# Kernel optimization log

Measured on AMD Instinct MI355X. Metric: run time of the kernel, lower is better.

Reference implementation:

```python
import jax, jax.numpy as jnp
import numpy as np

B, D = 128, 512
ORDER, DEPTH = 1, 2


def setup_inputs() -> dict:
    key = jax.random.key(0)
    kx, kw = jax.random.split(key)
    x = jax.random.normal(kx, (B, D), dtype=jnp.float32)
    # scale the cubic meta-weight so repeated contractions stay O(1)
    W = jax.random.normal(kw, (D, D, D), dtype=jnp.float32) * (1.0 / np.sqrt(D))
    bias = jnp.zeros((D,), dtype=jnp.float32)
    return {"x": x, "W": W, "bias": bias}


def reference(x, W, bias):
    # Meta-linear: per-sample effective weight obtained by contracting the
    # trailing `ORDER` modes of W (out, in, in, ...) with x, rescaled by
    # 1/sqrt(d) per contraction, then applied as a linear layer; repeat DEPTH times.
    sqrt_d = np.sqrt(x.shape[-1]).astype(np.float32)
    for _ in range(DEPTH):
        # first contraction introduces the batch dim: (out, in, k) x (b, k) -> (b, out, in)
        w = jnp.einsum('...k,bk->b...', W, x) / sqrt_d
        for _ in range(ORDER - 1):
            w = jnp.einsum('b...k,bk->b...', w, x) / sqrt_d
        x = jnp.einsum('boi,bi->bo', w, x) + bias
    return x
```

## Files before the change

### kernel.cpp

```cpp
#include <hip/hip_runtime.h>
#include <hip/hip_fp16.h>


typedef __attribute__((ext_vector_type(8))) _Float16 f16x8;
typedef __attribute__((ext_vector_type(4))) float    f32x4v;
typedef __attribute__((ext_vector_type(4))) unsigned u32x4;

#define DD 512
#define BB 128
#define INV_SQRT_D 0.04419417382415922f

static __device__ __forceinline__ unsigned pkh(float a, float b) {
    __half2 h = __float22half2_rn(make_float2(a, b));
    unsigned u;
    __builtin_memcpy(&u, &h, sizeof(u));
    return u;
}

static __device__ __forceinline__ u32x4 pack8s(f32x4v a, f32x4v b, float s) {
    u32x4 r;
    r.x = pkh(a.x * s, a.y * s);
    r.y = pkh(a.z * s, a.w * s);
    r.z = pkh(b.x * s, b.y * s);
    r.w = pkh(b.z * s, b.w * s);
    return r;
}

static __device__ __forceinline__ f16x8 as_h8(u32x4 q) {
    f16x8 v;
    __builtin_memcpy(&v, &q, sizeof(v));
    return v;
}

__global__ __launch_bounds__(256, 4)
void metagemm(const float* __restrict__ x, const float* __restrict__ W,
              float* __restrict__ acc) {
    __shared__ u32x4 Ab[2][1024];

    const int tid  = threadIdx.x;
    const int lane = tid & 63;
    const int wv   = tid >> 6;

    const int bid = blockIdx.x;
    const int ob  = bid >> 7;
    const int ig  = (bid >> 3) & 15;
    const int kp  = bid & 7;

    const int o0 = ob * 64 + wv * 16;
    const int i0 = ig * 32;
    const int kb = kp * 64;

    const int l15  = lane & 15;
    const int quad = lane >> 4;
    const int koff = quad * 8;

    const int bA = wv * 16 + l15;
    const int bB = (wv + 4) * 16 + l15;
    const float* xr0 = x + bA * DD + kb + koff;
    const float* xr1 = x + bB * DD + kb + koff;

    const int oW = o0 + l15;
    const float* wbase = W + (long)oW * (DD * DD) + kb + koff;

    f32x4v c[8];
#pragma unroll
    for (int f = 0; f < 8; ++f) c[f] = (f32x4v){0.f, 0.f, 0.f, 0.f};

    auto build = [&](int buf, int i) {
        const float s0 = x[bA * DD + i] * INV_SQRT_D;
        const float s1 = x[bB * DD + i] * INV_SQRT_D;
#pragma unroll
        for (int ks = 0; ks < 2; ++ks) {
            f32x4v a0 = *(const f32x4v*)(xr0 + ks * 32);
            f32x4v a1 = *(const f32x4v*)(xr0 + ks * 32 + 4);
            f32x4v b0 = *(const f32x4v*)(xr1 + ks * 32);
            f32x4v b1 = *(const f32x4v*)(xr1 + ks * 32 + 4);
            Ab[buf][(ks * 8 + wv) * 64 + lane]     = pack8s(a0, a1, s0);
            Ab[buf][(ks * 8 + wv + 4) * 64 + lane] = pack8s(b0, b1, s1);
        }
    };

    build(0, i0);
    __syncthreads();

#pragma unroll 1
    for (int n = 0; n < 32; ++n) {
        const int i   = i0 + n;
        const int buf = n & 1;

        const float* wp = wbase + i * DD;
        f32x4v wa = *(const f32x4v*)(wp);
        f32x4v wb = *(const f32x4v*)(wp + 4);
        f32x4v wc = *(const f32x4v*)(wp + 32);
        f32x4v wd = *(const f32x4v*)(wp + 36);

        if (n < 31) build(buf ^ 1, i + 1);

        f16x8 bf0 = as_h8(pack8s(wa, wb, 1.0f));
        f16x8 bf1 = as_h8(pack8s(wc, wd, 1.0f));

#pragma unroll
        for (int f = 0; f < 8; ++f) {
            f16x8 af = as_h8(Ab[buf][f * 64 + lane]);
            c[f] = __builtin_amdgcn_mfma_f32_16x16x32_f16(af, bf0, c[f], 0, 0, 0);
        }
#pragma unroll
        for (int f = 0; f < 8; ++f) {
            f16x8 af = as_h8(Ab[buf][(8 + f) * 64 + lane]);
            c[f] = __builtin_amdgcn_mfma_f32_16x16x32_f16(af, bf1, c[f], 0, 0, 0);
        }
        __syncthreads();
    }

    const int orow = o0 + l15;
    const int br0  = quad * 4;
#pragma unroll
    for (int f = 0; f < 8; ++f) {
#pragma unroll
        for (int r = 0; r < 4; ++r) {
            atomicAdd(&acc[(f * 16 + br0 + r) * DD + orow], c[f][r]);
        }
    }
}

__global__ void finalize(const float* __restrict__ acc, const float* __restrict__ bias,
                         float* __restrict__ out) {
    const int idx = blockIdx.x * 256 + threadIdx.x;
    out[idx] = acc[idx] + bias[idx & (DD - 1)];
}

extern "C" void kernel_launch(void* const* d_in, const int* in_sizes, int n_in,
                              void* d_out, int out_size, void* d_ws, size_t ws_size,
                              hipStream_t stream) {
    (void)in_sizes; (void)n_in; (void)out_size; (void)ws_size;

    const float* x    = (const float*)d_in[0];
    const float* W    = (const float*)d_in[1];
    const float* bias = (const float*)d_in[2];
    float* out = (float*)d_out;

    float* acc = (float*)d_ws;
    float* x1  = acc + BB * DD;

    hipMemsetAsync(acc, 0, BB * DD * sizeof(float), stream);
    metagemm<<<1024, 256, 0, stream>>>(x, W, acc);
    finalize<<<(BB * DD) / 256, 256, 0, stream>>>(acc, bias, x1);

    hipMemsetAsync(out, 0, BB * DD * sizeof(float), stream);
    metagemm<<<1024, 256, 0, stream>>>(x1, W, out);
    finalize<<<(BB * DD) / 256, 256, 0, stream>>>(out, bias, out);
}
```

Measured before the change: 1.023 ms.

## Precompute unscaled x tile once, scale per-i in registers, replace atomics with partials

```diff
diff --git a/kernel.cpp b/kernel.cpp
--- a/kernel.cpp
+++ b/kernel.cpp
@@ -12,121 +12,126 @@
 
 static __device__ __forceinline__ unsigned pkh(float a, float b) {
     __half2 h = __float22half2_rn(make_float2(a, b));
-    unsigned u;
-    __builtin_memcpy(&u, &h, sizeof(u));
-    return u;
+    unsigned u; __builtin_memcpy(&u, &h, sizeof(u)); return u;
 }
-
-static __device__ __forceinline__ u32x4 pack8s(f32x4v a, f32x4v b, float s) {
-    u32x4 r;
-    r.x = pkh(a.x * s, a.y * s);
-    r.y = pkh(a.z * s, a.w * s);
-    r.z = pkh(b.x * s, b.y * s);
-    r.w = pkh(b.z * s, b.w * s);
-    return r;
+static __device__ __forceinline__ u32x4 pack8(f32x4v a, f32x4v b) {
+    u32x4 r; r.x = pkh(a.x, a.y); r.y = pkh(a.z, a.w);
+             r.z = pkh(b.x, b.y); r.w = pkh(b.z, b.w); return r;
 }
-
 static __device__ __forceinline__ f16x8 as_h8(u32x4 q) {
-    f16x8 v;
-    __builtin_memcpy(&v, &q, sizeof(v));
-    return v;
+    f16x8 v; __builtin_memcpy(&v, &q, sizeof(v)); return v;
 }
 
 __global__ __launch_bounds__(256, 4)
 void metagemm(const float* __restrict__ x, const float* __restrict__ W,
-              float* __restrict__ acc) {
-    __shared__ u32x4 Ab[2][1024];
+              float* __restrict__ part) {
+    __shared__ u32x4    kp_lds[1024];
+    __shared__ unsigned sc_lds[4096];
 
     const int tid  = threadIdx.x;
     const int lane = tid & 63;
     const int wv   = tid >> 6;
+    const int bid  = blockIdx.x;
+    const int ob   = bid >> 7;
+    const int ig   = (bid >> 3) & 15;
+    const int kp   = bid & 7;
 
-    const int bid = blockIdx.x;
-    const int ob  = bid >> 7;
-    const int ig  = (bid >> 3) & 15;
-    const int kp  = bid & 7;
-
-    const int o0 = ob * 64 + wv * 16;
-    const int i0 = ig * 32;
-    const int kb = kp * 64;
-
+    const int o0   = ob * 64 + wv * 16;
+    const int i0   = ig * 32;
+    const int kb   = kp * 64;
     const int l15  = lane & 15;
     const int quad = lane >> 4;
     const int koff = quad * 8;
 
-    const int bA = wv * 16 + l15;
-    const int bB = (wv + 4) * 16 + l15;
-    const float* xr0 = x + bA * DD + kb + koff;
-    const float* xr1 = x + bB * DD + kb + koff;
+    const float* wbase = W + (long)(o0 + l15) * (DD * DD) + (long)i0 * DD + kb + koff;
 
-    const int oW = o0 + l15;
-    const float* wbase = W + (long)oW * (DD * DD) + kb + koff;
+    f32x4v wa = *(const f32x4v*)(wbase);
+    f32x4v wb = *(const f32x4v*)(wbase + 4);
+    f32x4v wc = *(const f32x4v*)(wbase + 32);
+    f32x4v wd = *(const f32x4v*)(wbase + 36);
+
+#pragma unroll
+    for (int ff = 0; ff < 2; ++ff) {
+        const int f   = wv * 2 + ff;
+        const int row = f * 16 + l15;
+        const float* xr = x + row * DD + kb + koff;
+#pragma unroll
+        for (int ks = 0; ks < 2; ++ks) {
+            f32x4v a = *(const f32x4v*)(xr + ks * 32);
+            f32x4v b = *(const f32x4v*)(xr + ks * 32 + 4);
+            kp_lds[(ks * 8 + f) * 64 + lane] = pack8(a, b);
+        }
+    }
+    {
+        const int row  = tid & 127;
+        const int half = tid >> 7;
+#pragma unroll
+        for (int c4 = 0; c4 < 4; ++c4) {
+            const int i = half * 16 + c4 * 4;
+            f32x4v v = *(const f32x4v*)(x + row * DD + i0 + i);
+#pragma unroll
+            for (int j = 0; j < 4; ++j) {
+                float s = v[j] * INV_SQRT_D;
+                sc_lds[(i + j) * 128 + row] = pkh(s, s);
+            }
+        }
+    }
+    __syncthreads();
 
     f32x4v c[8];
 #pragma unroll
     for (int f = 0; f < 8; ++f) c[f] = (f32x4v){0.f, 0.f, 0.f, 0.f};
 
-    auto build = [&](int buf, int i) {
-        const float s0 = x[bA * DD + i] * INV_SQRT_D;
-        const float s1 = x[bB * DD + i] * INV_SQRT_D;
-#pragma unroll
-        for (int ks = 0; ks < 2; ++ks) {
-            f32x4v a0 = *(const f32x4v*)(xr0 + ks * 32);
-            f32x4v a1 = *(const f32x4v*)(xr0 + ks * 32 + 4);
-            f32x4v b0 = *(const f32x4v*)(xr1 + ks * 32);
-            f32x4v b1 = *(const f32x4v*)(xr1 + ks * 32 + 4);
-            Ab[buf][(ks * 8 + wv) * 64 + lane]     = pack8s(a0, a1, s0);
-            Ab[buf][(ks * 8 + wv + 4) * 64 + lane] = pack8s(b0, b1, s1);
-        }
-    };
-
-    build(0, i0);
-    __syncthreads();
-
+    unsigned lic = 0;
 #pragma unroll 1
     for (int n = 0; n < 32; ++n) {
-        const int i   = i0 + n;
-        const int buf = n & 1;
+        asm volatile("" : "+v"(lic));
 
-        const float* wp = wbase + i * DD;
-        f32x4v wa = *(const f32x4v*)(wp);
-        f32x4v wb = *(const f32x4v*)(wp + 4);
-        f32x4v wc = *(const f32x4v*)(wp + 32);
-        f32x4v wd = *(const f32x4v*)(wp + 36);
+        f32x4v ca = wa, cb = wb, cc = wc, cd = wd;
+        if (n < 31) {
+            const float* wp = wbase + (n + 1) * DD;
+            wa = *(const f32x4v*)(wp);
+            wb = *(const f32x4v*)(wp + 4);
+            wc = *(const f32x4v*)(wp + 32);
+            wd = *(const f32x4v*)(wp + 36);
+        }
 
-        if (n < 31) build(buf ^ 1, i + 1);
+        f16x8 bf0 = as_h8(pack8(ca, cb));
+        f16x8 bf1 = as_h8(pack8(cc, cd));
 
-        f16x8 bf0 = as_h8(pack8s(wa, wb, 1.0f));
-        f16x8 bf1 = as_h8(pack8s(wc, wd, 1.0f));
+        const unsigned* scp = sc_lds + n * 128 + l15 + lic;
+        const u32x4*    kpp = kp_lds + lane + lic;
 
 #pragma unroll
         for (int f = 0; f < 8; ++f) {
-            f16x8 af = as_h8(Ab[buf][f * 64 + lane]);
-            c[f] = __builtin_amdgcn_mfma_f32_16x16x32_f16(af, bf0, c[f], 0, 0, 0);
+            unsigned su = scp[f * 16];
+            u32x4 sq = {su, su, su, su};
+            f16x8 sv = as_h8(sq);
+            f16x8 a0 = as_h8(kpp[f * 64]) * sv;
+            c[f] = __builtin_amdgcn_mfma_f32_16x16x32_f16(a0, bf0, c[f], 0, 0, 0);
+            f16x8 a1 = as_h8(kpp[(8 + f) * 64]) * sv;
+            c[f] = __builtin_amdgcn_mfma_f32_16x16x32_f16(a1, bf1, c[f], 0, 0, 0);
         }
-#pragma unroll
-        for (int f = 0; f < 8; ++f) {
-            f16x8 af = as_h8(Ab[buf][(8 + f) * 64 + lane]);
-            c[f] = __builtin_amdgcn_mfma_f32_16x16x32_f16(af, bf1, c[f], 0, 0, 0);
-        }
-        __syncthreads();
     }
 
-    const int orow = o0 + l15;
-    const int br0  = quad * 4;
+    float* pbase = part + (long)(ig * 8 + kp) * (BB * DD) + ob * 64;
+    const int ocol = wv * 16 + l15;
 #pragma unroll
     for (int f = 0; f < 8; ++f) {
 #pragma unroll
         for (int r = 0; r < 4; ++r) {
-            atomicAdd(&acc[(f * 16 + br0 + r) * DD + orow], c[f][r]);
+            pbase[(f * 16 + quad * 4 + r) * DD + ocol] = c[f][r];
         }
     }
 }
 
-__global__ void finalize(const float* __restrict__ acc, const float* __restrict__ bias,
-                         float* __restrict__ out) {
+__global__ void reduce_bias(const float* __restrict__ part, const float* __restrict__ bias,
+                            float* __restrict__ out) {
     const int idx = blockIdx.x * 256 + threadIdx.x;
-    out[idx] = acc[idx] + bias[idx & (DD - 1)];
+    float s = bias[idx & (DD - 1)];
+#pragma unroll 16
+    for (int p = 0; p < 128; ++p) s += part[(long)p * (BB * DD) + idx];
+    out[idx] = s;
 }
 
 extern "C" void kernel_launch(void* const* d_in, const int* in_sizes, int n_in,
@@ -139,14 +144,12 @@
     const float* bias = (const float*)d_in[2];
     float* out = (float*)d_out;
 
-    float* acc = (float*)d_ws;
-    float* x1  = acc + BB * DD;
+    float* part = (float*)d_ws;
+    float* x1   = part + 128 * BB * DD;
 
-    hipMemsetAsync(acc, 0, BB * DD * sizeof(float), stream);
-    metagemm<<<1024, 256, 0, stream>>>(x, W, acc);
-    finalize<<<(BB * DD) / 256, 256, 0, stream>>>(acc, bias, x1);
+    metagemm<<<1024, 256, 0, stream>>>(x, W, part);
+    reduce_bias<<<(BB * DD) / 256, 256, 0, stream>>>(part, bias, x1);
 
-    hipMemsetAsync(out, 0, BB * DD * sizeof(float), stream);
-    metagemm<<<1024, 256, 0, stream>>>(x1, W, out);
-    finalize<<<(BB * DD) / 256, 256, 0, stream>>>(out, bias, out);
+    metagemm<<<1024, 256, 0, stream>>>(x1, W, part);
+    reduce_bias<<<(BB * DD) / 256, 256, 0, stream>>>(part, bias, out);
 }
```

Measured after the change: 833.8 us. -18.5%, faster.
